# Optimization experiments

Measured on AMD Instinct MI355X. Metric: run time of the kernel, lower is better.

Reference implementation:

```python
import jax, jax.numpy as jnp
import numpy as np

EPS = 1e-5
N, A, CTX, H, E = 100000, 32, 5, 64, 1600000


def layer_norm(x, g, b):
    mu = x.mean(-1, keepdims=True)
    var = x.var(-1, keepdims=True)
    return (x - mu) / jnp.sqrt(var + EPS) * g + b


def batch_norm(x, g, b, m, v):
    # eval-mode BatchNorm with running stats
    return (x - m) / jnp.sqrt(v + EPS) * g + b


def gcn_conv(x, w, bias, src, dst, n):
    # src/dst already include self-loops; symmetric normalization D^-1/2 (A+I) D^-1/2
    h = x @ w
    deg = jax.ops.segment_sum(jnp.ones_like(src, dtype=x.dtype), dst, num_segments=n)
    inv_sqrt = jnp.where(deg > 0, 1.0 / jnp.sqrt(deg), 0.0)
    coef = inv_sqrt[src] * inv_sqrt[dst]  # [Etot]
    return jax.ops.segment_sum(h[src] * coef[:, None], dst, num_segments=n) + bias


def gat_conv(x, w, a_src, a_dst, bias, src, dst, n, heads, out_ch):
    h = (x @ w).reshape(n, heads, out_ch)           # [N,H,C]
    alpha_s = (h * a_src).sum(-1)                    # [N,H]
    alpha_d = (h * a_dst).sum(-1)                    # [N,H]
    e = jax.nn.leaky_relu(alpha_s[src] + alpha_d[dst], 0.2)  # [Etot,H]
    m = jax.ops.segment_max(e, dst, num_segments=n)  # segment softmax over incoming edges
    ex = jnp.exp(e - m[dst])
    s = jax.ops.segment_sum(ex, dst, num_segments=n)
    alpha = ex / (s[dst] + 1e-16)                    # [Etot,H]
    out = jax.ops.segment_sum(h[src] * alpha[..., None], dst, num_segments=n)
    return out.reshape(n, heads * out_ch) + bias


def setup_inputs() -> dict:
    key = jax.random.key(0)
    ks = iter(jax.random.split(key, 48))

    def rn(shape, scale=None):
        if scale is None:  # xavier-normal-ish
            fan_in, fan_out = (shape[0], shape[-1]) if len(shape) > 1 else (shape[0], shape[0])
            scale = float(np.sqrt(2.0 / (fan_in + fan_out)))
        return jax.random.normal(next(ks), shape, jnp.float32) * scale

    inp = {
        "accessibility_features": jax.random.normal(next(ks), (N, A), jnp.float32),
        "context_features": jax.random.normal(next(ks), (N, CTX), jnp.float32),
        "edge_index": jax.random.randint(next(ks), (2, E), 0, N, jnp.int32),
        # context gate
        "cg_w1": rn((CTX, 32)), "cg_b1": jnp.zeros((32,), jnp.float32),
        "cg_w2": rn((32, 32)), "cg_b2": jnp.zeros((32,), jnp.float32),
        "cg_aw": rn((32, A)), "cg_ab": jnp.zeros((A,), jnp.float32),
        "base_imp": jnp.ones((A,), jnp.float32),
        # input LayerNorm
        "ln_g": jnp.ones((A,), jnp.float32), "ln_b": jnp.zeros((A,), jnp.float32),
        # feature encoder
        "fe_w1": rn((A, H)), "fe_b1": jnp.zeros((H,), jnp.float32),
        "fe_w2": rn((H, H)), "fe_b2": jnp.zeros((H,), jnp.float32),
        # GCN1 + BN1
        "gcn1_w": rn((H, H)), "gcn1_b": jnp.zeros((H,), jnp.float32),
        "bn1_g": 1.0 + rn((H,), 0.05), "bn1_b": rn((H,), 0.05),
        "bn1_m": rn((H,), 0.05), "bn1_v": 1.0 + jax.random.uniform(next(ks), (H,), jnp.float32) * 0.1,
        # GAT (heads=2, out=32) + BN2
        "gat_w": rn((H, H)), "gat_asrc": rn((2, 32), 0.1), "gat_adst": rn((2, 32), 0.1),
        "gat_b": jnp.zeros((H,), jnp.float32),
        "bn2_g": 1.0 + rn((H,), 0.05), "bn2_b": rn((H,), 0.05),
        "bn2_m": rn((H,), 0.05), "bn2_v": 1.0 + jax.random.uniform(next(ks), (H,), jnp.float32) * 0.1,
        # GCN2 + BN3
        "gcn2_w": rn((H, H // 2)), "gcn2_b": jnp.zeros((H // 2,), jnp.float32),
        "bn3_g": 1.0 + rn((H // 2,), 0.05), "bn3_b": rn((H // 2,), 0.05),
        "bn3_m": rn((H // 2,), 0.05), "bn3_v": 1.0 + jax.random.uniform(next(ks), (H // 2,), jnp.float32) * 0.1,
        # SVI predictor head
        "sp_w1": rn((H // 2, H // 4)), "sp_b1": jnp.zeros((H // 4,), jnp.float32),
        "sp_w2": rn((H // 4, 1)), "sp_b2": jnp.zeros((1,), jnp.float32),
    }
    return inp


def reference(accessibility_features, context_features, edge_index,
              cg_w1, cg_b1, cg_w2, cg_b2, cg_aw, cg_ab, base_imp,
              ln_g, ln_b, fe_w1, fe_b1, fe_w2, fe_b2,
              gcn1_w, gcn1_b, bn1_g, bn1_b, bn1_m, bn1_v,
              gat_w, gat_asrc, gat_adst, gat_b, bn2_g, bn2_b, bn2_m, bn2_v,
              gcn2_w, gcn2_b, bn3_g, bn3_b, bn3_m, bn3_v,
              sp_w1, sp_b1, sp_w2, sp_b2):
    n = accessibility_features.shape[0]
    loops = jnp.arange(n, dtype=edge_index.dtype)
    src = jnp.concatenate([edge_index[0], loops])
    dst = jnp.concatenate([edge_index[1], loops])

    # context-gated feature modulation
    ce = jax.nn.relu(context_features @ cg_w1 + cg_b1) @ cg_w2 + cg_b2
    attw = jax.nn.softmax(ce @ cg_aw + cg_ab, axis=-1)
    x = layer_norm(accessibility_features * (attw * base_imp), ln_g, ln_b)

    # dense feature encoder (dropout = identity in eval)
    x = jax.nn.relu(jax.nn.relu(x @ fe_w1 + fe_b1) @ fe_w2 + fe_b2)

    x = jax.nn.relu(batch_norm(gcn_conv(x, gcn1_w, gcn1_b, src, dst, n), bn1_g, bn1_b, bn1_m, bn1_v))
    x = jax.nn.relu(batch_norm(gat_conv(x, gat_w, gat_asrc, gat_adst, gat_b, src, dst, n, 2, 32), bn2_g, bn2_b, bn2_m, bn2_v))
    x = jax.nn.relu(batch_norm(gcn_conv(x, gcn2_w, gcn2_b, src, dst, n), bn3_g, bn3_b, bn3_m, bn3_v))

    svi = jax.nn.sigmoid((jax.nn.relu(x @ sp_w1 + sp_b1) @ sp_w2 + sp_b2).squeeze(-1))
    return svi
```

## Files before the change

kernel.cpp:

```cpp
#include <hip/hip_runtime.h>
#include <hip/hip_bf16.h>

constexpr int A_DIM = 32;
constexpr int CTX_DIM = 5;
constexpr float EPS = 1e-5f;
constexpr int BCAP = 4096;
constexpr int EPB = 8192;
constexpr int NBP = 800;

__device__ __forceinline__ float lrelu02(float x) { return x > 0.f ? x : 0.2f * x; }

__device__ __forceinline__ unsigned int f2bf_bits(float x) {
    __hip_bfloat16 h = __float2bfloat16(x);
    return (unsigned int)reinterpret_cast<unsigned short&>(h);
}
__device__ __forceinline__ float bf_lo(unsigned int v) { return __uint_as_float(v << 16); }
__device__ __forceinline__ float bf_hi(unsigned int v) { return __uint_as_float(v & 0xffff0000u); }

__global__ __launch_bounds__(256) void k_bucketA(const int* __restrict__ ei, int E,
                                                 int* __restrict__ bcnt,
                                                 int* __restrict__ bstage, int NB) {
    __shared__ int hist[NBP];
    __shared__ int hexcl[NBP];
    __shared__ int cur[NBP];
    __shared__ int sd[256];
    __shared__ int stg[EPB];
    int tid = threadIdx.x;
    int base = blockIdx.x * EPB;
    int cnt = min(EPB, E - base);
    if (cnt <= 0) return;
    for (int i = tid; i < NBP; i += 256) hist[i] = 0;
    __syncthreads();
    for (int i = tid; i < cnt; i += 256) atomicAdd(&hist[ei[E + base + i] >> 7], 1);
    __syncthreads();
    {
        int idx0 = tid * 4;
        int v[4];
        int s = 0;
#pragma unroll
        for (int j = 0; j < 4; j++) {
            int idx = idx0 + j;
            v[j] = (idx < NB) ? hist[idx] : 0;
            s += v[j];
        }
        sd[tid] = s;
        __syncthreads();
        for (int off = 1; off < 256; off <<= 1) {
            int t = (tid >= off) ? sd[tid - off] : 0;
            __syncthreads();
            sd[tid] += t;
            __syncthreads();
        }
        int run = tid ? sd[tid - 1] : 0;
#pragma unroll
        for (int j = 0; j < 4; j++) {
            int idx = idx0 + j;
            if (idx < NBP) {
                hexcl[idx] = run;
                cur[idx] = run;
            }
            run += v[j];
        }
    }
    __syncthreads();
    for (int i = tid; i < cnt; i += 256) {
        int s = ei[base + i];
        int d = ei[E + base + i];
        int b = d >> 7;
        int pos = atomicAdd(&cur[b], 1);
        stg[pos] = ((d & 127) << 17) | s;
    }
    __syncthreads();
    for (int b = tid; b < NB; b += 256) {
        int c = hist[b];
        if (!c) continue;
        int gpos = atomicAdd(&bcnt[b * 16], c);
        int lim = min(c, BCAP - gpos);
        int lb = hexcl[b];
        int* dstp = bstage + (size_t)b * BCAP + gpos;
        for (int j = 0; j < lim; j++) dstp[j] = stg[lb + j];
    }
}

__global__ void k_bscan(const int* __restrict__ bcnt, int nb, int* __restrict__ bbase,
                        int* __restrict__ rowp, int n, int E) {
    __shared__ int sd[256];
    int tid = threadIdx.x;
    int run = 0;
    for (int base = 0; base < nb; base += 256) {
        int idx = base + tid;
        int v = (idx < nb) ? min(bcnt[idx * 16], BCAP) : 0;
        sd[tid] = v;
        __syncthreads();
        for (int off = 1; off < 256; off <<= 1) {
            int t = (tid >= off) ? sd[tid - off] : 0;
            __syncthreads();
            sd[tid] += t;
            __syncthreads();
        }
        if (idx < nb) bbase[idx] = run + sd[tid] - v;
        run += sd[255];
        __syncthreads();
    }
    if (tid == 0) rowp[n] = run;
}

__global__ __launch_bounds__(256) void k_bucketB(
    const int* __restrict__ bstage, const int* __restrict__ bcnt, const int* __restrict__ bbase,
    int* __restrict__ rowp, float* __restrict__ inv, int* __restrict__ csrc, int n) {
    __shared__ int scur[128];
    __shared__ int sstage[BCAP];
    int b = blockIdx.x, tid = threadIdx.x;
    int base_node = b << 7;
    int nn = min(128, n - base_node);
    int cntE = min(bcnt[b * 16], BCAP);
    int ebase = bbase[b];
    const int* st = bstage + (size_t)b * BCAP;
    if (tid < 128) scur[tid] = 0;
    __syncthreads();
    for (int i = tid; i < cntE; i += 256) atomicAdd(&scur[st[i] >> 17], 1);
    __syncthreads();
    int deg = (tid < 128) ? scur[tid] : 0;
    __syncthreads();
    if (tid < 128) scur[tid] = deg;
    __syncthreads();
    for (int off = 1; off < 128; off <<= 1) {
        int t = (tid >= off && tid < 128) ? scur[tid - off] : 0;
        __syncthreads();
        if (tid < 128) scur[tid] += t;
        __syncthreads();
    }
    int excl = (tid < 128) ? (scur[tid] - deg) : 0;
    if (tid < nn) {
        rowp[base_node + tid] = ebase + excl;
        inv[base_node + tid] = rsqrtf((float)deg + 1.0f);
    }
    if (tid < 128) scur[tid] = excl;
    __syncthreads();
    for (int i = tid; i < cntE; i += 256) {
        int p = st[i];
        int pos = atomicAdd(&scur[p >> 17], 1);
        sstage[pos] = p & 0x1FFFF;
    }
    __syncthreads();
    for (int i = tid; i < cntE; i += 256) csrc[ebase + i] = sstage[i];
}

__global__ __launch_bounds__(256) void k_gate(
    const float* __restrict__ accf, const float* __restrict__ ctxf,
    const float* __restrict__ w1, const float* __restrict__ b1,
    const float* __restrict__ w2, const float* __restrict__ b2,
    const float* __restrict__ aw, const float* __restrict__ ab,
    const float* __restrict__ base_imp, const float* __restrict__ lng,
    const float* __restrict__ lnb, float* __restrict__ xn_out, int n) {
    __shared__ float sh[4][64];
    int tid = threadIdx.x, wid = tid >> 6, lane = tid & 63;
    int l = lane & 31, half = lane >> 5;
    float w1c[CTX_DIM], w2c[32], awc[32];
#pragma unroll
    for (int k = 0; k < CTX_DIM; k++) w1c[k] = w1[k * 32 + l];
#pragma unroll
    for (int k = 0; k < 32; k++) w2c[k] = w2[k * 32 + l];
#pragma unroll
    for (int k = 0; k < 32; k++) awc[k] = aw[k * 32 + l];
    float b1v = b1[l], b2v = b2[l], abv = ab[l], bimp = base_imp[l];
    float lngv = lng[l], lnbv = lnb[l];
    float* s0 = sh[wid];
    const float4* s4 = (const float4*)s0;

    int npairs = (n + 1) >> 1;
    int gw = blockIdx.x * 4 + wid, nw = gridDim.x * 4;
    for (int pair = gw; pair < npairs; pair += nw) {
        int node = pair * 2 + half;
        bool valid = node < n;
        float cx0 = 0, cx1 = 0, cx2 = 0, cx3 = 0, cx4 = 0, xa = 0;
        if (valid) {
            cx0 = ctxf[node * CTX_DIM + 0];
            cx1 = ctxf[node * CTX_DIM + 1];
            cx2 = ctxf[node * CTX_DIM + 2];
            cx3 = ctxf[node * CTX_DIM + 3];
            cx4 = ctxf[node * CTX_DIM + 4];
            xa = accf[node * A_DIM + l];
        }
        float h1 = b1v + cx0 * w1c[0] + cx1 * w1c[1] + cx2 * w1c[2] + cx3 * w1c[3] + cx4 * w1c[4];
        s0[lane] = fmaxf(h1, 0.f);
        {
            float a0 = 0, a1 = 0, a2 = 0, a3 = 0;
#pragma unroll
            for (int k = 0; k < 8; k++) {
                float4 t = s4[half * 8 + k];
                a0 += t.x * w2c[4 * k];
                a1 += t.y * w2c[4 * k + 1];
                a2 += t.z * w2c[4 * k + 2];
                a3 += t.w * w2c[4 * k + 3];
            }
            s0[lane] = b2v + ((a0 + a1) + (a2 + a3));
        }
        float z;
        {
            float a0 = 0, a1 = 0, a2 = 0, a3 = 0;
#pragma unroll
            for (int k = 0; k < 8; k++) {
                float4 t = s4[half * 8 + k];
                a0 += t.x * awc[4 * k];
                a1 += t.y * awc[4 * k + 1];
                a2 += t.z * awc[4 * k + 2];
                a3 += t.w * awc[4 * k + 3];
            }
            z = abv + ((a0 + a1) + (a2 + a3));
        }
        float m = z;
#pragma unroll
        for (int off = 16; off; off >>= 1) m = fmaxf(m, __shfl_xor(m, off, 64));
        float ex = __expf(z - m);
        float ss = ex;
#pragma unroll
        for (int off = 16; off; off >>= 1) ss += __shfl_xor(ss, off, 64);
        float v = xa * (ex / ss) * bimp;
        float s1 = v, s2 = v * v;
#pragma unroll
        for (int off = 16; off; off >>= 1) {
            s1 += __shfl_xor(s1, off, 64);
            s2 += __shfl_xor(s2, off, 64);
        }
        float mu = s1 * (1.f / 32.f);
        float var = s2 * (1.f / 32.f) - mu * mu;
        float xn = (v - mu) * rsqrtf(var + EPS) * lngv + lnbv;
        if (valid) xn_out[(size_t)node * 32 + l] = xn;
    }
}

__global__ __launch_bounds__(256) void k_encode(
    const float* __restrict__ xn, const float* __restrict__ fw1, const float* __restrict__ fb1,
    const float* __restrict__ fw2, const float* __restrict__ fb2, float* __restrict__ xout,
    int n) {
    __shared__ float sh[4][128];
    int tid = threadIdx.x, wid = tid >> 6, lane = tid & 63;
    float f1c[32], f2c[64];
#pragma unroll
    for (int k = 0; k < 32; k++) f1c[k] = fw1[k * 64 + lane];
#pragma unroll
    for (int k = 0; k < 64; k++) f2c[k] = fw2[k * 64 + lane];
    float fb1v = fb1[lane], fb2v = fb2[lane];
    float* s0 = sh[wid];
    const float4* s4 = (const float4*)s0;

    int npairs = (n + 1) >> 1;
    int gw = blockIdx.x * 4 + wid, nw = gridDim.x * 4;
    int total = n * 32;
    for (int pair = gw; pair < npairs; pair += nw) {
        int idx = pair * 64 + lane;
        s0[lane] = (idx < total) ? xn[idx] : 0.f;
        float u0, u1;
        {
            float a0 = 0, a1 = 0, b0 = 0, b1 = 0;
#pragma unroll
            for (int k = 0; k < 8; k++) {
                float4 t = s4[k];
                float4 t2 = s4[8 + k];
                a0 += t.x * f1c[4 * k] + t.y * f1c[4 * k + 1];
                a1 += t.z * f1c[4 * k + 2] + t.w * f1c[4 * k + 3];
                b0 += t2.x * f1c[4 * k] + t2.y * f1c[4 * k + 1];
                b1 += t2.z * f1c[4 * k + 2] + t2.w * f1c[4 * k + 3];
            }
            u0 = fmaxf(fb1v + a0 + a1, 0.f);
            u1 = fmaxf(fb1v + b0 + b1, 0.f);
        }
        s0[lane] = u0;
        s0[64 + lane] = u1;
        float o0, o1;
        {
            float a0 = 0, a1 = 0, b0 = 0, b1 = 0;
#pragma unroll
            for (int k = 0; k < 16; k++) {
                float4 t = s4[k];
                float4 t2 = s4[16 + k];
                a0 += t.x * f2c[4 * k] + t.y * f2c[4 * k + 1];
                a1 += t.z * f2c[4 * k + 2] + t.w * f2c[4 * k + 3];
                b0 += t2.x * f2c[4 * k] + t2.y * f2c[4 * k + 1];
                b1 += t2.z * f2c[4 * k + 2] + t2.w * f2c[4 * k + 3];
            }
            o0 = fmaxf(fb2v + a0 + a1, 0.f);
            o1 = fmaxf(fb2v + b0 + b1, 0.f);
        }
        int n0 = pair * 2;
        xout[(size_t)n0 * 64 + lane] = o0;
        if (n0 + 1 < n) xout[(size_t)(n0 + 1) * 64 + lane] = o1;
    }
}

template <int COUT, bool DO_ATTN, bool SCALE>
__global__ __launch_bounds__(256) void k_transform(
    const float* __restrict__ x, const float* __restrict__ w,
    const float* __restrict__ asrc, const float* __restrict__ adst,
    const float* __restrict__ inv, __hip_bfloat16* __restrict__ h,
    float* __restrict__ attn, int n) {
    constexpr int NPG = 64 / COUT;
    __shared__ __align__(16) float scr[4][NPG * 64];
    int tid = threadIdx.x, wid = tid >> 6, lane = tid & 63;
    int ch = lane % COUT;
    int sub = lane / COUT;
    float wr[64];
#pragma unroll
    for (int k = 0; k < 64; k++) wr[k] = w[k * COUT + ch];
    float as_r = 0.f, ad_r = 0.f;
    if (DO_ATTN) {
        as_r = asrc[lane];
        ad_r = adst[lane];
    }
    int ngroups = (n + NPG - 1) / NPG;
    int gw = blockIdx.x * 4 + wid, nw = gridDim.x * 4;
    int total = n * 64;
    unsigned int* h2 = (unsigned int*)h;
    for (int g = gw; g < ngroups; g += nw) {
        int base = g * NPG * 64;
#pragma unroll
        for (int i = 0; i < NPG; i++) {
            int idx = i * 64 + lane;
            scr[wid][idx] = (base + idx < total) ? x[base + idx] : 0.f;
        }
        float acc0 = 0.f, acc1 = 0.f;
        const float4* sp4 = (const float4*)(&scr[wid][sub * 64]);
#pragma unroll
        for (int k = 0; k < 16; k++) {
            float4 t = sp4[k];
            acc0 += t.x * wr[4 * k] + t.y * wr[4 * k + 1];
            acc1 += t.z * wr[4 * k + 2] + t.w * wr[4 * k + 3];
        }
        float acc = acc0 + acc1;
        int node = g * NPG + sub;
        if (SCALE) acc *= (node < n) ? inv[node] : 0.f;
        unsigned int mine = f2bf_bits(acc);
        unsigned int oth = (unsigned int)__shfl_xor((int)mine, 1, 64);
        if ((ch & 1) == 0 && node < n)
            h2[(size_t)node * (COUT / 2) + (ch >> 1)] = mine | (oth << 16);
        if (DO_ATTN) {
            float ps = acc * as_r, pd = acc * ad_r;
#pragma unroll
            for (int off = 16; off; off >>= 1) {
                ps += __shfl_xor(ps, off, 64);
                pd += __shfl_xor(pd, off, 64);
            }
            if ((lane & 31) == 0 && node < n) {
                int hd = lane >> 5;
                attn[node * 4 + hd] = ps;
                attn[node * 4 + 2 + hd] = pd;
            }
        }
    }
}

template <int C>
__global__ __launch_bounds__(256) void k_gcn_agg(
    const __hip_bfloat16* __restrict__ h, const int* __restrict__ rowp,
    const int* __restrict__ csrc, const float* __restrict__ inv,
    const float* __restrict__ bias, const float* __restrict__ bg,
    const float* __restrict__ bb, const float* __restrict__ bm,
    const float* __restrict__ bv, float* __restrict__ out, int n, int dummy) {
    constexpr int LPE = C / 2;
    constexpr int NE = 64 / LPE;
    int tid = threadIdx.x, lane = tid & 63;
    int node = blockIdx.x * 4 + (tid >> 6);
    if (node >= n) return;
    float invd = inv[node];
    int e0 = rowp[node], e1 = rowp[node + 1];
    int l = lane & (LPE - 1);
    int grp = lane / LPE;
    const unsigned int* h2 = (const unsigned int*)h;
    float acc0 = 0.f, acc1 = 0.f;
    for (int cb = e0; cb < e1; cb += 64) {
        int kn = min(64, e1 - cb);
        int s_l = (lane < kn) ? csrc[cb + lane] : dummy;
        for (int kb = 0; kb < kn; kb += NE * 8) {
            unsigned int v[8];
#pragma unroll
            for (int i = 0; i < 8; i++) {
                int k = kb + i * NE + grp;
                int s = __shfl(s_l, k, 64);
                v[i] = h2[(size_t)s * LPE + l];
            }
#pragma unroll
            for (int i = 0; i < 8; i++) {
                acc0 += bf_lo(v[i]);
                acc1 += bf_hi(v[i]);
            }
        }
    }
#pragma unroll
    for (int off = LPE; off < 64; off <<= 1) {
        acc0 += __shfl_xor(acc0, off, 64);
        acc1 += __shfl_xor(acc1, off, 64);
    }
    unsigned int sv = h2[(size_t)node * LPE + l];
    acc0 = (acc0 + bf_lo(sv)) * invd;
    acc1 = (acc1 + bf_hi(sv)) * invd;
    if (grp == 0) {
        int c0 = 2 * l;
        float sc0 = bg[c0] * rsqrtf(bv[c0] + EPS);
        float sc1 = bg[c0 + 1] * rsqrtf(bv[c0 + 1] + EPS);
        float r0 = (acc0 + bias[c0] - bm[c0]) * sc0 + bb[c0];
        float r1 = (acc1 + bias[c0 + 1] - bm[c0 + 1]) * sc1 + bb[c0 + 1];
        ((float2*)out)[(size_t)node * LPE + l] = make_float2(fmaxf(r0, 0.f), fmaxf(r1, 0.f));
    }
}

__global__ __launch_bounds__(256) void k_gat_agg(
    const __hip_bfloat16* __restrict__ h, const int* __restrict__ rowp,
    const int* __restrict__ csrc, const float* __restrict__ attn,
    const float* __restrict__ bias, const float* __restrict__ bg,
    const float* __restrict__ bb, const float* __restrict__ bm,
    const float* __restrict__ bv, float* __restrict__ out, int n) {
    __shared__ uint2 sed[4][64];
    int tid = threadIdx.x, lane = tid & 63, wid = tid >> 6;
    int node = blockIdx.x * 4 + wid;
    if (node >= n) return;
    uint2* se = sed[wid];
    const float4* a4p = (const float4*)attn;
    float4 ad = a4p[node];
    float ad0 = ad.z, ad1 = ad.w;
    float es0 = lrelu02(ad.x + ad0), es1 = lrelu02(ad.y + ad1);
    int e0 = rowp[node], e1 = rowp[node + 1];
    int deg = e1 - e0;
    int kn0 = min(deg, 64);
    int s_l = (lane < kn0) ? csrc[e0 + lane] : node;
    float4 a_l = a4p[s_l];
    float l0 = (lane < kn0) ? lrelu02(a_l.x + ad0) : -3.4e38f;
    float l1 = (lane < kn0) ? lrelu02(a_l.y + ad1) : -3.4e38f;
    float m0 = fmaxf(l0, es0), m1 = fmaxf(l1, es1);
    for (int cb = e0 + 64; cb < e1; cb += 64) {
        if (cb + lane < e1) {
            float4 a = a4p[csrc[cb + lane]];
            m0 = fmaxf(m0, lrelu02(a.x + ad0));
            m1 = fmaxf(m1, lrelu02(a.y + ad1));
        }
    }
#pragma unroll
    for (int off = 32; off; off >>= 1) {
        m0 = fmaxf(m0, __shfl_xor(m0, off, 64));
        m1 = fmaxf(m1, __shfl_xor(m1, off, 64));
    }
    float ex0 = (lane < kn0) ? __expf(l0 - m0) : 0.f;
    float ex1 = (lane < kn0) ? __expf(l1 - m1) : 0.f;
    float t0 = ex0, t1 = ex1;
    se[lane] = make_uint2((unsigned int)s_l, f2bf_bits(ex0) | (f2bf_bits(ex1) << 16));
    int l = lane & 31, grp = lane >> 5;
    bool hd2 = l >= 16;
    const unsigned int* h2 = (const unsigned int*)h;
    float acc0 = 0.f, acc1 = 0.f;
    for (int kb = 0; kb < kn0; kb += 16) {
        unsigned int v[8];
        float wg[8];
#pragma unroll
        for (int i = 0; i < 8; i++) {
            int k = kb + i * 2 + grp;
            uint2 e = se[k];
            wg[i] = hd2 ? bf_hi(e.y) : bf_lo(e.y);
            v[i] = h2[(size_t)e.x * 32 + l];
        }
#pragma unroll
        for (int i = 0; i < 8; i++) {
            acc0 += wg[i] * bf_lo(v[i]);
            acc1 += wg[i] * bf_hi(v[i]);
        }
    }
    for (int cb = e0 + 64; cb < e1; cb += 64) {
        int kn = min(64, e1 - cb);
        int s_c = (lane < kn) ? csrc[cb + lane] : node;
        float4 a_c = a4p[s_c];
        float c0 = (lane < kn) ? __expf(lrelu02(a_c.x + ad0) - m0) : 0.f;
        float c1 = (lane < kn) ? __expf(lrelu02(a_c.y + ad1) - m1) : 0.f;
        t0 += c0;
        t1 += c1;
        se[lane] = make_uint2((unsigned int)s_c, f2bf_bits(c0) | (f2bf_bits(c1) << 16));
        for (int kb = 0; kb < kn; kb += 16) {
            unsigned int v[8];
            float wg[8];
#pragma unroll
            for (int i = 0; i < 8; i++) {
                int k = kb + i * 2 + grp;
                uint2 e = se[k];
                wg[i] = hd2 ? bf_hi(e.y) : bf_lo(e.y);
                v[i] = h2[(size_t)e.x * 32 + l];
            }
#pragma unroll
            for (int i = 0; i < 8; i++) {
                acc0 += wg[i] * bf_lo(v[i]);
                acc1 += wg[i] * bf_hi(v[i]);
            }
        }
    }
#pragma unroll
    for (int off = 32; off; off >>= 1) {
        t0 += __shfl_xor(t0, off, 64);
        t1 += __shfl_xor(t1, off, 64);
    }
    t0 += __expf(es0 - m0);
    t1 += __expf(es1 - m1);
    acc0 += __shfl_xor(acc0, 32, 64);
    acc1 += __shfl_xor(acc1, 32, 64);
    unsigned int sv = h2[(size_t)node * 32 + l];
    float ws = hd2 ? __expf(es1 - m1) : __expf(es0 - m0);
    acc0 += ws * bf_lo(sv);
    acc1 += ws * bf_hi(sv);
    float rsh = hd2 ? (1.f / (t1 + 1e-16f)) : (1.f / (t0 + 1e-16f));
    acc0 *= rsh;
    acc1 *= rsh;
    if (grp == 0) {
        int c0 = 2 * l;
        float sc0 = bg[c0] * rsqrtf(bv[c0] + EPS);
        float sc1 = bg[c0 + 1] * rsqrtf(bv[c0 + 1] + EPS);
        float r0 = (acc0 + bias[c0] - bm[c0]) * sc0 + bb[c0];
        float r1 = (acc1 + bias[c0 + 1] - bm[c0 + 1]) * sc1 + bb[c0 + 1];
        ((float2*)out)[(size_t)node * 32 + l] = make_float2(fmaxf(r0, 0.f), fmaxf(r1, 0.f));
    }
}

__global__ __launch_bounds__(256) void k_head(
    const float* __restrict__ x, const float* __restrict__ w1, const float* __restrict__ b1,
    const float* __restrict__ w2, const float* __restrict__ b2, float* __restrict__ out, int n) {
    __shared__ float sw1[512], sb1[16], sw2[16];
    __shared__ float sb2v;
    __shared__ float scr[4][64];
    int tid = threadIdx.x;
    for (int i = tid; i < 512; i += 256) sw1[i] = w1[i];
    if (tid < 16) {
        sb1[tid] = b1[tid];
        sw2[tid] = w2[tid];
    }
    if (tid == 0) sb2v = b2[0];
    __syncthreads();
    int wid = tid >> 6, lane = tid & 63;
    int half = lane >> 5;
    int np = (n + 1) >> 1;
    int gw = blockIdx.x * 4 + wid, nw = gridDim.x * 4;
    int total = n * 32;
    for (int g = gw; g < np; g += nw) {
        int idx = g * 64 + lane;
        scr[wid][lane] = (idx < total) ? x[idx] : 0.f;
        int j = lane & 15;
        float u = sb1[j];
#pragma unroll
        for (int k = 0; k < 32; k++) u += scr[wid][half * 32 + k] * sw1[k * 16 + j];
        u = fmaxf(u, 0.f);
        float p = u * sw2[j];
#pragma unroll
        for (int off = 8; off; off >>= 1) p += __shfl_xor(p, off, 64);
        int node = g * 2 + half;
        if ((lane & 31) == 0 && node < n) {
            float z = p + sb2v;
            out[node] = 1.f / (1.f + __expf(-z));
        }
    }
}

extern "C" void kernel_launch(void* const* d_in, const int* in_sizes, int n_in,
                              void* d_out, int out_size, void* d_ws, size_t ws_size,
                              hipStream_t stream) {
    const float* accf = (const float*)d_in[0];
    const float* ctxf = (const float*)d_in[1];
    const int* ei = (const int*)d_in[2];
    const float* cg_w1 = (const float*)d_in[3];
    const float* cg_b1 = (const float*)d_in[4];
    const float* cg_w2 = (const float*)d_in[5];
    const float* cg_b2 = (const float*)d_in[6];
    const float* cg_aw = (const float*)d_in[7];
    const float* cg_ab = (const float*)d_in[8];
    const float* base_imp = (const float*)d_in[9];
    const float* ln_g = (const float*)d_in[10];
    const float* ln_b = (const float*)d_in[11];
    const float* fe_w1 = (const float*)d_in[12];
    const float* fe_b1 = (const float*)d_in[13];
    const float* fe_w2 = (const float*)d_in[14];
    const float* fe_b2 = (const float*)d_in[15];
    const float* gcn1_w = (const float*)d_in[16];
    const float* gcn1_b = (const float*)d_in[17];
    const float* bn1_g = (const float*)d_in[18];
    const float* bn1_b = (const float*)d_in[19];
    const float* bn1_m = (const float*)d_in[20];
    const float* bn1_v = (const float*)d_in[21];
    const float* gat_w = (const float*)d_in[22];
    const float* gat_asrc = (const float*)d_in[23];
    const float* gat_adst = (const float*)d_in[24];
    const float* gat_b = (const float*)d_in[25];
    const float* bn2_g = (const float*)d_in[26];
    const float* bn2_b = (const float*)d_in[27];
    const float* bn2_m = (const float*)d_in[28];
    const float* bn2_v = (const float*)d_in[29];
    const float* gcn2_w = (const float*)d_in[30];
    const float* gcn2_b = (const float*)d_in[31];
    const float* bn3_g = (const float*)d_in[32];
    const float* bn3_b = (const float*)d_in[33];
    const float* bn3_m = (const float*)d_in[34];
    const float* bn3_v = (const float*)d_in[35];
    const float* sp_w1 = (const float*)d_in[36];
    const float* sp_b1 = (const float*)d_in[37];
    const float* sp_w2 = (const float*)d_in[38];
    const float* sp_b2 = (const float*)d_in[39];

    int n = in_sizes[0] / A_DIM;
    int E = in_sizes[2] / 2;
    int NB = (n + 127) >> 7;

    char* p = (char*)d_ws;
    auto alloc = [&](size_t bytes) -> void* {
        void* r = (void*)p;
        p += (bytes + 255) & ~(size_t)255;
        return r;
    };
    float* X = (float*)alloc((size_t)n * 64 * 4);
    __hip_bfloat16* Hb = (__hip_bfloat16*)alloc((size_t)n * 64 * 2 + 256);
    float* attn = (float*)alloc((size_t)n * 4 * 4);
    float* XN = (float*)alloc((size_t)n * 32 * 4);
    int* rowp = (int*)alloc((size_t)(n + 1) * 4);
    float* inv = (float*)alloc((size_t)n * 4);
    int* csrc = (int*)alloc((size_t)E * 4);
    int* bcnt = (int*)alloc((size_t)NB * 16 * 4);
    int* bbase = (int*)alloc((size_t)NB * 4);
    int* bstage = (int*)alloc((size_t)NB * BCAP * 4);

    hipMemsetAsync(bcnt, 0, (size_t)NB * 16 * 4, stream);
    hipMemsetAsync((char*)Hb + (size_t)128 * n, 0, 192, stream);
    k_bucketA<<<(E + EPB - 1) / EPB, 256, 0, stream>>>(ei, E, bcnt, bstage, NB);
    k_bscan<<<1, 256, 0, stream>>>(bcnt, NB, bbase, rowp, n, E);
    k_bucketB<<<NB, 256, 0, stream>>>(bstage, bcnt, bbase, rowp, inv, csrc, n);

    k_gate<<<1024, 256, 0, stream>>>(accf, ctxf, cg_w1, cg_b1, cg_w2, cg_b2, cg_aw, cg_ab,
                                     base_imp, ln_g, ln_b, XN, n);
    k_encode<<<1024, 256, 0, stream>>>(XN, fe_w1, fe_b1, fe_w2, fe_b2, X, n);
    k_transform<64, false, true><<<1024, 256, 0, stream>>>(X, gcn1_w, nullptr, nullptr, inv, Hb,
                                                           nullptr, n);
    k_gcn_agg<64><<<(n + 3) / 4, 256, 0, stream>>>(Hb, rowp, csrc, inv, gcn1_b, bn1_g, bn1_b,
                                                   bn1_m, bn1_v, X, n, n);
    k_transform<64, true, false><<<1024, 256, 0, stream>>>(X, gat_w, gat_asrc, gat_adst, nullptr,
                                                           Hb, attn, n);
    k_gat_agg<<<(n + 3) / 4, 256, 0, stream>>>(Hb, rowp, csrc, attn, gat_b, bn2_g, bn2_b, bn2_m,
                                               bn2_v, X, n);
    k_transform<32, false, true><<<1024, 256, 0, stream>>>(X, gcn2_w, nullptr, nullptr, inv, Hb,
                                                           nullptr, n);
    k_gcn_agg<32><<<(n + 3) / 4, 256, 0, stream>>>(Hb, rowp, csrc, inv, gcn2_b, bn3_g, bn3_b,
                                                   bn3_m, bn3_v, X, n, 2 * n + 2);
    k_head<<<512, 256, 0, stream>>>(X, sp_w1, sp_b1, sp_w2, sp_b2, (float*)d_out, n);
}
```

Before: 363.0 us.

## Drop GAT softmax max pass and fold bucket scan into bucketB

The GAT aggregation no longer computes the per-node segment max. It exponentiates clamped logits directly, which removes an extra gather pass over the neighbors and a wave reduction. The clamp at 60 guards against overflow, but without max subtraction the result relies on logits staying in a safe range and can differ from the reference for extreme inputs. Separately, the single-block bucket prefix scan kernel is removed. Each bucketB block now sums the preceding bucket counts itself, which saves a kernel launch and a serial dependency at the cost of redundant reads.

Result: faster. 351.5 us (-3.2%).

```diff
diff --git a/kernel.cpp b/kernel.cpp
--- a/kernel.cpp
+++ b/kernel.cpp
@@ -82,40 +82,27 @@
     }
 }
 
-__global__ void k_bscan(const int* __restrict__ bcnt, int nb, int* __restrict__ bbase,
-                        int* __restrict__ rowp, int n, int E) {
-    __shared__ int sd[256];
-    int tid = threadIdx.x;
-    int run = 0;
-    for (int base = 0; base < nb; base += 256) {
-        int idx = base + tid;
-        int v = (idx < nb) ? min(bcnt[idx * 16], BCAP) : 0;
-        sd[tid] = v;
-        __syncthreads();
-        for (int off = 1; off < 256; off <<= 1) {
-            int t = (tid >= off) ? sd[tid - off] : 0;
-            __syncthreads();
-            sd[tid] += t;
-            __syncthreads();
-        }
-        if (idx < nb) bbase[idx] = run + sd[tid] - v;
-        run += sd[255];
-        __syncthreads();
-    }
-    if (tid == 0) rowp[n] = run;
-}
-
 __global__ __launch_bounds__(256) void k_bucketB(
-    const int* __restrict__ bstage, const int* __restrict__ bcnt, const int* __restrict__ bbase,
-    int* __restrict__ rowp, float* __restrict__ inv, int* __restrict__ csrc, int n) {
+    const int* __restrict__ bstage, const int* __restrict__ bcnt, int* __restrict__ rowp,
+    float* __restrict__ inv, int* __restrict__ csrc, int n, int NB) {
     __shared__ int scur[128];
+    __shared__ int sred[256];
     __shared__ int sstage[BCAP];
     int b = blockIdx.x, tid = threadIdx.x;
+    int part = 0;
+    for (int i = tid; i < b; i += 256) part += min(bcnt[i * 16], BCAP);
+    sred[tid] = part;
+    __syncthreads();
+    for (int off = 128; off; off >>= 1) {
+        if (tid < off) sred[tid] += sred[tid + off];
+        __syncthreads();
+    }
+    int ebase = sred[0];
     int base_node = b << 7;
     int nn = min(128, n - base_node);
     int cntE = min(bcnt[b * 16], BCAP);
-    int ebase = bbase[b];
     const int* st = bstage + (size_t)b * BCAP;
+    if (b == NB - 1 && tid == 0) rowp[n] = ebase + cntE;
     if (tid < 128) scur[tid] = 0;
     __syncthreads();
     for (int i = tid; i < cntE; i += 256) atomicAdd(&scur[st[i] >> 17], 1);
@@ -418,29 +405,15 @@
     const float4* a4p = (const float4*)attn;
     float4 ad = a4p[node];
     float ad0 = ad.z, ad1 = ad.w;
-    float es0 = lrelu02(ad.x + ad0), es1 = lrelu02(ad.y + ad1);
+    float exs0 = __expf(fminf(lrelu02(ad.x + ad0), 60.f));
+    float exs1 = __expf(fminf(lrelu02(ad.y + ad1), 60.f));
     int e0 = rowp[node], e1 = rowp[node + 1];
     int deg = e1 - e0;
     int kn0 = min(deg, 64);
     int s_l = (lane < kn0) ? csrc[e0 + lane] : node;
     float4 a_l = a4p[s_l];
-    float l0 = (lane < kn0) ? lrelu02(a_l.x + ad0) : -3.4e38f;
-    float l1 = (lane < kn0) ? lrelu02(a_l.y + ad1) : -3.4e38f;
-    float m0 = fmaxf(l0, es0), m1 = fmaxf(l1, es1);
-    for (int cb = e0 + 64; cb < e1; cb += 64) {
-        if (cb + lane < e1) {
-            float4 a = a4p[csrc[cb + lane]];
-            m0 = fmaxf(m0, lrelu02(a.x + ad0));
-            m1 = fmaxf(m1, lrelu02(a.y + ad1));
-        }
-    }
-#pragma unroll
-    for (int off = 32; off; off >>= 1) {
-        m0 = fmaxf(m0, __shfl_xor(m0, off, 64));
-        m1 = fmaxf(m1, __shfl_xor(m1, off, 64));
-    }
-    float ex0 = (lane < kn0) ? __expf(l0 - m0) : 0.f;
-    float ex1 = (lane < kn0) ? __expf(l1 - m1) : 0.f;
+    float ex0 = (lane < kn0) ? __expf(fminf(lrelu02(a_l.x + ad0), 60.f)) : 0.f;
+    float ex1 = (lane < kn0) ? __expf(fminf(lrelu02(a_l.y + ad1), 60.f)) : 0.f;
     float t0 = ex0, t1 = ex1;
     se[lane] = make_uint2((unsigned int)s_l, f2bf_bits(ex0) | (f2bf_bits(ex1) << 16));
     int l = lane & 31, grp = lane >> 5;
@@ -467,8 +440,8 @@
         int kn = min(64, e1 - cb);
         int s_c = (lane < kn) ? csrc[cb + lane] : node;
         float4 a_c = a4p[s_c];
-        float c0 = (lane < kn) ? __expf(lrelu02(a_c.x + ad0) - m0) : 0.f;
-        float c1 = (lane < kn) ? __expf(lrelu02(a_c.y + ad1) - m1) : 0.f;
+        float c0 = (lane < kn) ? __expf(fminf(lrelu02(a_c.x + ad0), 60.f)) : 0.f;
+        float c1 = (lane < kn) ? __expf(fminf(lrelu02(a_c.y + ad1), 60.f)) : 0.f;
         t0 += c0;
         t1 += c1;
         se[lane] = make_uint2((unsigned int)s_c, f2bf_bits(c0) | (f2bf_bits(c1) << 16));
@@ -494,12 +467,12 @@
         t0 += __shfl_xor(t0, off, 64);
         t1 += __shfl_xor(t1, off, 64);
     }
-    t0 += __expf(es0 - m0);
-    t1 += __expf(es1 - m1);
+    t0 += exs0;
+    t1 += exs1;
     acc0 += __shfl_xor(acc0, 32, 64);
     acc1 += __shfl_xor(acc1, 32, 64);
     unsigned int sv = h2[(size_t)node * 32 + l];
-    float ws = hd2 ? __expf(es1 - m1) : __expf(es0 - m0);
+    float ws = hd2 ? exs1 : exs0;
     acc0 += ws * bf_lo(sv);
     acc1 += ws * bf_hi(sv);
     float rsh = hd2 ? (1.f / (t1 + 1e-16f)) : (1.f / (t0 + 1e-16f));
@@ -615,14 +588,12 @@
     float* inv = (float*)alloc((size_t)n * 4);
     int* csrc = (int*)alloc((size_t)E * 4);
     int* bcnt = (int*)alloc((size_t)NB * 16 * 4);
-    int* bbase = (int*)alloc((size_t)NB * 4);
     int* bstage = (int*)alloc((size_t)NB * BCAP * 4);
 
     hipMemsetAsync(bcnt, 0, (size_t)NB * 16 * 4, stream);
     hipMemsetAsync((char*)Hb + (size_t)128 * n, 0, 192, stream);
     k_bucketA<<<(E + EPB - 1) / EPB, 256, 0, stream>>>(ei, E, bcnt, bstage, NB);
-    k_bscan<<<1, 256, 0, stream>>>(bcnt, NB, bbase, rowp, n, E);
-    k_bucketB<<<NB, 256, 0, stream>>>(bstage, bcnt, bbase, rowp, inv, csrc, n);
+    k_bucketB<<<NB, 256, 0, stream>>>(bstage, bcnt, rowp, inv, csrc, n, NB);
 
     k_gate<<<1024, 256, 0, stream>>>(accf, ctxf, cg_w1, cg_b1, cg_w2, cg_b2, cg_aw, cg_ab,
                                      base_imp, ln_g, ln_b, XN, n);
```
